# Optimization experiments

Measured on AMD Instinct MI355X. Metric: run time of the kernel, lower is better.

The kernel has to match this reference:

```python
import jax, jax.numpy as jnp
import numpy as np
import math

D_MODEL = 1024
N_HEADS = 16
HEAD_DIM = D_MODEL // N_HEADS


def get_slopes(n_heads: int) -> jnp.ndarray:
    def pow2_slopes(n):
        start = 2.0 ** (-8.0 / n)
        return np.array([start * start ** i for i in range(n)], dtype=np.float32)
    if math.log2(n_heads).is_integer():
        return jnp.asarray(pow2_slopes(n_heads))
    closest = 2 ** math.floor(math.log2(n_heads))
    base = pow2_slopes(closest)
    extra = pow2_slopes(2 * closest)[::2][: n_heads - closest]
    return jnp.asarray(np.concatenate([base, extra]))


def setup_inputs() -> dict:
    key = jax.random.key(0)
    ks = jax.random.split(key, 9)
    s = 1.0 / math.sqrt(D_MODEL)
    x = jax.random.normal(ks[0], (2, 2048, D_MODEL), dtype=jnp.float32)
    q_w = jax.random.uniform(ks[1], (D_MODEL, D_MODEL), jnp.float32, -s, s)
    q_b = jax.random.uniform(ks[2], (D_MODEL,), jnp.float32, -s, s)
    k_w = jax.random.uniform(ks[3], (D_MODEL, D_MODEL), jnp.float32, -s, s)
    k_b = jax.random.uniform(ks[4], (D_MODEL,), jnp.float32, -s, s)
    v_w = jax.random.uniform(ks[5], (D_MODEL, D_MODEL), jnp.float32, -s, s)
    v_b = jax.random.uniform(ks[6], (D_MODEL,), jnp.float32, -s, s)
    o_w = jax.random.uniform(ks[7], (D_MODEL, D_MODEL), jnp.float32, -s, s)
    o_b = jax.random.uniform(ks[8], (D_MODEL,), jnp.float32, -s, s)
    return {"x": x, "q_w": q_w, "q_b": q_b, "k_w": k_w, "k_b": k_b,
            "v_w": v_w, "v_b": v_b, "o_w": o_w, "o_b": o_b}


def reference(x, q_w, q_b, k_w, k_b, v_w, v_b, o_w, o_b):
    B, S, D = x.shape
    H, hd = N_HEADS, HEAD_DIM
    # torch Linear: y = x @ W.T + b
    Q = (x @ q_w.T + q_b).reshape(B, S, H, hd).transpose(0, 2, 1, 3)  # [B,H,S,hd]
    K = (x @ k_w.T + k_b).reshape(B, S, H, hd).transpose(0, 2, 1, 3)
    V = (x @ v_w.T + v_b).reshape(B, S, H, hd).transpose(0, 2, 1, 3)
    scores = jnp.einsum('bhqd,bhkd->bhqk', Q, K) / math.sqrt(hd)
    # ALiBi bias: slopes[h] * (k_pos - q_pos)
    pos = jnp.arange(S)
    rel = (pos[None, :] - pos[:, None]).astype(scores.dtype)  # [S,S]
    slopes = get_slopes(H)
    scores = scores + slopes[None, :, None, None] * rel[None, None, :, :]
    # causal mask
    causal = pos[None, :] <= pos[:, None]  # [S,S] True where allowed
    scores = jnp.where(causal[None, None], scores, -jnp.inf)
    attn = jax.nn.softmax(scores, axis=-1)  # dropout=0 (eval)
    out = jnp.einsum('bhqk,bhkd->bhqd', attn, V)
    out = out.transpose(0, 2, 1, 3).reshape(B, S, D)
    return out @ o_w.T + o_b
```

## Files before the change

### kernel.cpp

```cpp
#include <hip/hip_runtime.h>
#include <hip/hip_bf16.h>

typedef __attribute__((ext_vector_type(8))) short short8;
typedef __attribute__((ext_vector_type(4))) float float4v;
typedef __attribute__((ext_vector_type(4))) short short4v;
typedef __attribute__((ext_vector_type(4))) unsigned int uint4v;
typedef __attribute__((ext_vector_type(2))) unsigned int uint2v;

#define B_ 2
#define S_ 2048
#define D_ 1024
#define H_ 16
#define HD_ 64
#define M_ 4096
#define LOG2E 1.442695040888963f

__device__ __forceinline__ unsigned short f2bf(float f) {
  unsigned int u = __builtin_bit_cast(unsigned int, f);
  u += 0x7fffu + ((u >> 16) & 1u);
  return (unsigned short)(u >> 16);
}

__device__ __forceinline__ unsigned int pkbf(float a, float b) {
  __hip_bfloat162 h = __float22bfloat162_rn(make_float2(a, b));
  unsigned int u;
  __builtin_memcpy(&u, &h, sizeof(u));
  return u;
}

__device__ __forceinline__ void gload_lds16(const void* g, void* l) {
  __builtin_amdgcn_global_load_lds(
      (const __attribute__((address_space(1))) void*)g,
      (__attribute__((address_space(3))) void*)l, 16, 0, 0);
}

__global__ __launch_bounds__(256, 4) void cvt_kernel(
    const float* __restrict__ x,  const float* __restrict__ qw,
    const float* __restrict__ kw, const float* __restrict__ vw,
    const float* __restrict__ ow, unsigned short* __restrict__ dst)
{
  const int seg = blockIdx.y;
  const float* src;
  size_t doff;
  if (seg < 4)       { src = x + (size_t)seg * 1048576; doff = (size_t)seg * 1048576; }
  else if (seg == 4) { src = qw; doff = 4194304u; }
  else if (seg == 5) { src = kw; doff = 4194304u + 1048576u; }
  else if (seg == 6) { src = vw; doff = 4194304u + 2097152u; }
  else               { src = ow; doff = 4194304u + 3145728u; }
  const size_t i = ((size_t)blockIdx.x * 256 + threadIdx.x) * 4;
  float4v v = *(const float4v*)(src + i);
  short4v p;
#pragma unroll
  for (int r = 0; r < 4; ++r) p[r] = (short)f2bf(v[r]);
  *(short4v*)(dst + doff + i) = p;
}

template <int TN>
__global__ __launch_bounds__(256, 2) void gemm_kernel(
    const unsigned short* __restrict__ X,
    const unsigned short* __restrict__ W0, const unsigned short* __restrict__ W1,
    const unsigned short* __restrict__ W2,
    const float* __restrict__ Bi0, const float* __restrict__ Bi1,
    const float* __restrict__ Bi2,
    unsigned short* O0, unsigned short* O1, unsigned short* O2,
    float* OutF, int md0, int md1, int md2)
{
  constexpr int NJ = TN / 32;
  const int z = blockIdx.z;
  const unsigned short* W  = (z == 0) ? W0  : ((z == 1) ? W1  : W2);
  const float* Bi          = (z == 0) ? Bi0 : ((z == 1) ? Bi1 : Bi2);
  unsigned short* Out      = (z == 0) ? O0  : ((z == 1) ? O1  : O2);
  const int mode           = (z == 0) ? md0 : ((z == 1) ? md1 : md2);

  __shared__ __align__(16) char smem[8192 + TN * 64];
  __shared__ __align__(16) float tb[32 * 132];
  char* As = smem;
  char* Bs = smem + 8192;

  const int t = threadIdx.x, l = t & 63;
  const int w = t >> 6, lr = l & 15, lg = l >> 4;
  const int n0 = blockIdx.x * TN, m0 = blockIdx.y * 128;
  const int wm = (w >> 1) * 64, wn = (w & 1) * (TN / 2);

  float4v acc[4][NJ];
#pragma unroll
  for (int i = 0; i < 4; ++i)
#pragma unroll
    for (int j = 0; j < NJ; ++j) acc[i][j] = (float4v){0.f, 0.f, 0.f, 0.f};

  const int c0 = t, c1 = t + 256;
  const int r0 = c0 >> 2, k80 = (c0 & 3) * 8;
  const int r1 = c1 >> 2, k81 = (c1 & 3) * 8;

  for (int k0 = 0; k0 < 1024; k0 += 32) {
    __syncthreads();
    gload_lds16(X + (size_t)(m0 + r0) * 1024 + k0 + k80, As + c0 * 16);
    gload_lds16(X + (size_t)(m0 + r1) * 1024 + k0 + k81, As + c1 * 16);
    gload_lds16(W + (size_t)(n0 + r0) * 1024 + k0 + k80, Bs + c0 * 16);
    if (TN == 128)
      gload_lds16(W + (size_t)(n0 + r1) * 1024 + k0 + k81, Bs + c1 * 16);
    __syncthreads();

    short8 af[4], bfr[NJ];
#pragma unroll
    for (int i = 0; i < 4; ++i)
      af[i] = *(const short8*)(As + (wm + i * 16 + lr) * 64 + lg * 16);
#pragma unroll
    for (int j = 0; j < NJ; ++j)
      bfr[j] = *(const short8*)(Bs + (wn + j * 16 + lr) * 64 + lg * 16);
#pragma unroll
    for (int i = 0; i < 4; ++i)
#pragma unroll
      for (int j = 0; j < NJ; ++j)
        acc[i][j] = __builtin_amdgcn_mfma_f32_16x16x32_bf16(af[i], bfr[j], acc[i][j], 0, 0, 0);
  }

  float bv[NJ];
#pragma unroll
  for (int j = 0; j < NJ; ++j) bv[j] = Bi[n0 + wn + j * 16 + lr];

  if constexpr (TN == 128) {
    if (mode == 1) {
      const int rbase = (w >> 1) * 16;
      const int row16 = t >> 3, chunk = t & 7;
#pragma unroll
      for (int i = 0; i < 4; ++i) {
#pragma unroll
        for (int j = 0; j < 4; ++j)
#pragma unroll
          for (int r = 0; r < 4; ++r)
            tb[(rbase + lg * 4 + r) * 132 + wn + j * 16 + lr] = acc[i][j][r] + bv[j];
        __syncthreads();
        const int grow = m0 + ((row16 < 16) ? (i * 16 + row16) : (64 + i * 16 + row16 - 16));
        const int b = grow >> 11, sl = grow & 2047;
        const int colg = n0 + chunk * 16;
        const int hh = colg >> 6, d0 = colg & 63;
        float4v v4[4];
#pragma unroll
        for (int q = 0; q < 4; ++q)
          v4[q] = *(const float4v*)(tb + row16 * 132 + chunk * 16 + q * 4);
        uint4v lo, hi;
#pragma unroll
        for (int q = 0; q < 2; ++q) {
          lo[q * 2]     = pkbf(v4[q][0], v4[q][1]);
          lo[q * 2 + 1] = pkbf(v4[q][2], v4[q][3]);
          hi[q * 2]     = pkbf(v4[q + 2][0], v4[q + 2][1]);
          hi[q * 2 + 1] = pkbf(v4[q + 2][2], v4[q + 2][3]);
        }
        unsigned short* dst = Out + ((size_t)(b * H_ + hh) * S_ + sl) * HD_ + d0;
        *(short8*)dst = __builtin_bit_cast(short8, lo);
        *(short8*)(dst + 8) = __builtin_bit_cast(short8, hi);
        __syncthreads();
      }
      return;
    }
    if (mode == 2) {
#pragma unroll
      for (int i = 0; i < 4; ++i) {
        const int rowb = m0 + wm + i * 16 + lg * 4;
#pragma unroll
        for (int j = 0; j < 4; ++j) {
          const int col = n0 + wn + j * 16 + lr;
          const int b = rowb >> 11, s = rowb & 2047;
          const int hh = col >> 6, d = col & 63;
          uint2v pk2;
          pk2[0] = pkbf(acc[i][j][0] + bv[j], acc[i][j][1] + bv[j]);
          pk2[1] = pkbf(acc[i][j][2] + bv[j], acc[i][j][3] + bv[j]);
          *(short4v*)(Out + ((size_t)(b * H_ + hh) * HD_ + d) * S_ + s) =
              __builtin_bit_cast(short4v, pk2);
        }
      }
      return;
    }
  }
#pragma unroll
  for (int i = 0; i < 4; ++i) {
    const int rowb = m0 + wm + i * 16 + lg * 4;
#pragma unroll
    for (int j = 0; j < NJ; ++j) {
      const int col = n0 + wn + j * 16 + lr;
#pragma unroll
      for (int r = 0; r < 4; ++r)
        OutF[(size_t)(rowb + r) * 1024 + col] = acc[i][j][r] + bv[j];
    }
  }
}

__global__ __launch_bounds__(256, 2) void attn_kernel(
    const unsigned short* __restrict__ Q, const unsigned short* __restrict__ K,
    const unsigned short* __restrict__ VT, unsigned short* __restrict__ O)
{
  __shared__ __align__(16) char smem[32768];

  const int t = threadIdx.x, l = t & 63;
  const int w = t >> 6, lr = l & 15, lg = l >> 4;
  const int bh = blockIdx.x;
  const int it = 31 - (int)blockIdx.y;
  const int h = bh & 15;

  const unsigned short* qbp = Q + (size_t)bh * S_ * HD_;
  const unsigned short* kbp = K + (size_t)bh * S_ * HD_;
  const unsigned short* vbp = VT + (size_t)bh * HD_ * S_;

  const float slope2 = __builtin_amdgcn_exp2f(-0.5f * (float)(h + 1)) * LOG2E;
  const float qksc = 0.125f * LOG2E;

  const int g0 = t, g1 = t + 256;
  const int sr0 = g0 >> 3, sc0 = (g0 & 7) ^ (sr0 & 7);
  const int sr1 = g1 >> 3, sc1 = (g1 & 7) ^ (sr1 & 7);

  const int fchunk = ((4 + lg) ^ (lr & 7)) * 16;
  const int fchunk0 = ((lg) ^ (lr & 7)) * 16;

  const int qrow = it * 64 + w * 16;
  const int qpos = qrow + lr;

  short8 ones;
#pragma unroll
  for (int e = 0; e < 8; ++e) ones[e] = (short)0x3F80;

  short8 qf[2];
#pragma unroll
  for (int ks = 0; ks < 2; ++ks)
    qf[ks] = *(const short8*)(qbp + (size_t)(qrow + lr) * HD_ + ks * 32 + lg * 8);

  float4v o_acc[4], l_acc;
#pragma unroll
  for (int dt = 0; dt < 4; ++dt) o_acc[dt] = (float4v){0.f, 0.f, 0.f, 0.f};
  l_acc = (float4v){0.f, 0.f, 0.f, 0.f};
  float m_st = -1e30f;

  gload_lds16(kbp + (size_t)sr0 * HD_ + sc0 * 8, smem + g0 * 16);
  gload_lds16(kbp + (size_t)sr1 * HD_ + sc1 * 8, smem + g1 * 16);
  gload_lds16(vbp + (size_t)sr0 * S_ + sc0 * 8, smem + 16384 + g0 * 16);
  gload_lds16(vbp + (size_t)sr1 * S_ + sc1 * 8, smem + 16384 + g1 * 16);
  __syncthreads();

  for (int j = 0; j <= it; ++j) {
    const int cur = j & 1;
    char* Ks = smem + (cur ? 8192 : 0);
    char* Vs = smem + 16384 + (cur ? 8192 : 0);
    if (j < it) {
      char* Kn = smem + (cur ? 0 : 8192);
      char* Vn = smem + 16384 + (cur ? 0 : 8192);
      const int jn = j + 1;
      gload_lds16(kbp + (size_t)(jn * 64 + sr0) * HD_ + sc0 * 8, Kn + g0 * 16);
      gload_lds16(kbp + (size_t)(jn * 64 + sr1) * HD_ + sc1 * 8, Kn + g1 * 16);
      gload_lds16(vbp + (size_t)sr0 * S_ + jn * 64 + sc0 * 8, Vn + g0 * 16);
      gload_lds16(vbp + (size_t)sr1 * S_ + jn * 64 + sc1 * 8, Vn + g1 * 16);
    }

    float4v s_acc[4];
#pragma unroll
    for (int nj = 0; nj < 4; ++nj) {
      s_acc[nj] = (float4v){0.f, 0.f, 0.f, 0.f};
      short8 kf0 = *(const short8*)(Ks + (nj * 16 + lr) * 128 + fchunk0);
      s_acc[nj] = __builtin_amdgcn_mfma_f32_16x16x32_bf16(kf0, qf[0], s_acc[nj], 0, 0, 0);
      short8 kf1 = *(const short8*)(Ks + (nj * 16 + lr) * 128 + fchunk);
      s_acc[nj] = __builtin_amdgcn_mfma_f32_16x16x32_bf16(kf1, qf[1], s_acc[nj], 0, 0, 0);
    }

#pragma unroll
    for (int nj = 0; nj < 4; ++nj) {
      const float cb = slope2 * (float)(j * 64 + nj * 16 + lg * 4);
#pragma unroll
      for (int r = 0; r < 4; ++r)
        s_acc[nj][r] = s_acc[nj][r] * qksc + (cb + slope2 * (float)r);
    }
    if (j == it) {
#pragma unroll
      for (int nj = 0; nj < 4; ++nj)
#pragma unroll
        for (int r = 0; r < 4; ++r) {
          const int kpos = j * 64 + nj * 16 + lg * 4 + r;
          if (kpos > qpos) s_acc[nj][r] = -1e30f;
        }
    }

    float mx = s_acc[0][0];
#pragma unroll
    for (int nj = 0; nj < 4; ++nj)
#pragma unroll
      for (int r = 0; r < 4; ++r) mx = fmaxf(mx, s_acc[nj][r]);
    mx = fmaxf(mx, __shfl_xor(mx, 16, 64));
    mx = fmaxf(mx, __shfl_xor(mx, 32, 64));
    const float mn = fmaxf(m_st, mx);
    const float alpha = __builtin_amdgcn_exp2f(m_st - mn);
    m_st = mn;
#pragma unroll
    for (int nj = 0; nj < 4; ++nj)
#pragma unroll
      for (int r = 0; r < 4; ++r)
        s_acc[nj][r] = __builtin_amdgcn_exp2f(s_acc[nj][r] - mn);
#pragma unroll
    for (int dt = 0; dt < 4; ++dt)
#pragma unroll
      for (int r = 0; r < 4; ++r) o_acc[dt][r] *= alpha;
#pragma unroll
    for (int r = 0; r < 4; ++r) l_acc[r] *= alpha;

    short8 pT[2];
#pragma unroll
    for (int njp = 0; njp < 2; ++njp) {
      uint4v u;
      u[0] = pkbf(s_acc[njp * 2][0], s_acc[njp * 2][1]);
      u[1] = pkbf(s_acc[njp * 2][2], s_acc[njp * 2][3]);
      u[2] = pkbf(s_acc[njp * 2 + 1][0], s_acc[njp * 2 + 1][1]);
      u[3] = pkbf(s_acc[njp * 2 + 1][2], s_acc[njp * 2 + 1][3]);
      pT[njp] = __builtin_bit_cast(short8, u);
    }

    l_acc = __builtin_amdgcn_mfma_f32_16x16x32_bf16(ones, pT[0], l_acc, 0, 0, 0);
    l_acc = __builtin_amdgcn_mfma_f32_16x16x32_bf16(ones, pT[1], l_acc, 0, 0, 0);

    const int vcl = lr & 7;
#pragma unroll
    for (int dt = 0; dt < 4; ++dt) {
      const char* rowp = Vs + (dt * 16 + lr) * 128;
#pragma unroll
      for (int njp = 0; njp < 2; ++njp) {
        const int cA = ((njp * 4 + (lg >> 1)) ^ vcl) * 16 + (lg & 1) * 8;
        const int cB = ((njp * 4 + 2 + (lg >> 1)) ^ vcl) * 16 + (lg & 1) * 8;
        short4v v0 = *(const short4v*)(rowp + cA);
        short4v v1 = *(const short4v*)(rowp + cB);
        short8 vf8;
#pragma unroll
        for (int e = 0; e < 4; ++e) { vf8[e] = v0[e]; vf8[e + 4] = v1[e]; }
        o_acc[dt] = __builtin_amdgcn_mfma_f32_16x16x32_bf16(vf8, pT[njp], o_acc[dt], 0, 0, 0);
      }
    }
    __syncthreads();
  }

  char* tw = smem + w * 4416;
#pragma unroll
  for (int dt = 0; dt < 4; ++dt)
#pragma unroll
    for (int r = 0; r < 4; ++r)
      *(float*)(tw + ((dt * 16 + lg * 4 + r) * 17 + lr) * 4) = o_acc[dt][r];
  if (lg == 0) *(float*)(tw + 4352 + lr * 4) = l_acc[0];

  const int q2 = l >> 2, dbase = (l & 3) * 16;
  const float invl = 1.0f / *(const float*)(tw + 4352 + q2 * 4);
  uint4v os0, os1;
#pragma unroll
  for (int k = 0; k < 8; ++k) {
    const float va = *(const float*)(tw + ((dbase + 2 * k) * 17 + q2) * 4) * invl;
    const float vb = *(const float*)(tw + ((dbase + 2 * k + 1) * 17 + q2) * 4) * invl;
    if (k < 4) os0[k] = pkbf(va, vb); else os1[k - 4] = pkbf(va, vb);
  }
  const int brow = (bh >> 4) * S_;
  unsigned short* op = O + (size_t)(brow + qrow + q2) * 1024 + h * 64 + dbase;
  *(short8*)op = __builtin_bit_cast(short8, os0);
  *(short8*)(op + 8) = __builtin_bit_cast(short8, os1);
}

extern "C" void kernel_launch(void* const* d_in, const int* in_sizes, int n_in,
                              void* d_out, int out_size, void* d_ws, size_t ws_size,
                              hipStream_t stream) {
  (void)in_sizes; (void)n_in; (void)out_size; (void)ws_size;
  const float* x  = (const float*)d_in[0];
  const float* qw = (const float*)d_in[1];
  const float* qb = (const float*)d_in[2];
  const float* kw = (const float*)d_in[3];
  const float* kb = (const float*)d_in[4];
  const float* vw = (const float*)d_in[5];
  const float* vb = (const float*)d_in[6];
  const float* ow = (const float*)d_in[7];
  const float* ob = (const float*)d_in[8];
  float* out = (float*)d_out;

  unsigned short* xb  = (unsigned short*)d_ws;
  unsigned short* qwb = xb  + (size_t)M_ * D_;
  unsigned short* kwb = qwb + (size_t)D_ * D_;
  unsigned short* vwb = kwb + (size_t)D_ * D_;
  unsigned short* owb = vwb + (size_t)D_ * D_;
  unsigned short* qws = owb + (size_t)D_ * D_;
  unsigned short* kws = qws + (size_t)M_ * D_;
  unsigned short* vws = kws + (size_t)M_ * D_;
  unsigned short* aws = vws + (size_t)M_ * D_;

  cvt_kernel<<<dim3(1024, 8), dim3(256), 0, stream>>>(x, qw, kw, vw, ow, xb);
  gemm_kernel<128><<<dim3(8, 32, 3), dim3(256), 0, stream>>>(
      xb, qwb, kwb, vwb, qb, kb, vb, qws, kws, vws, out, 1, 1, 2);
  attn_kernel<<<dim3(32, 32), dim3(256), 0, stream>>>(qws, kws, vws, aws);
  gemm_kernel<64><<<dim3(16, 32, 1), dim3(256), 0, stream>>>(
      aws, owb, owb, owb, ob, ob, ob, aws, aws, aws, out, 0, 0, 0);
}
```

Before: 185.3 us.

## Lazy softmax rescale, hoisted ALiBi bias, permuted V layout for 16-byte loads

The V projection epilogue now permutes sequence positions within each 32-key group, so the attention loop can read each V fragment with one 16-byte LDS load instead of two 8-byte loads plus a register shuffle. The per-block ALiBi bias is hoisted into a precomputed per-lane table plus a running offset that is folded into the running max. Rescaling of the output and denominator accumulators is skipped unless some lane's max grows by more than a threshold, in the style of FA4 lazy rescaling. The max reduction uses three-input max ops. The lazy rescale adds a wave-level vote and a branch, and it relies on a bounded exp2 growth for fp32 and bf16 range safety.

```diff
diff --git a/kernel.cpp b/kernel.cpp
--- a/kernel.cpp
+++ b/kernel.cpp
@@ -26,6 +26,10 @@
   unsigned int u;
   __builtin_memcpy(&u, &h, sizeof(u));
   return u;
+}
+
+__device__ __forceinline__ float max3f(float a, float b, float c) {
+  return fmaxf(fmaxf(a, b), c);
 }
 
 __device__ __forceinline__ void gload_lds16(const void* g, void* l) {
@@ -163,10 +167,13 @@
           const int col = n0 + wn + j * 16 + lr;
           const int b = rowb >> 11, s = rowb & 2047;
           const int hh = col >> 6, d = col & 63;
+          const int gI = (s >> 2) & 7;
+          const int gP = ((gI & 3) << 1) | (gI >> 2);
+          const int sN = (s & ~31) | (gP << 2);
           uint2v pk2;
           pk2[0] = pkbf(acc[i][j][0] + bv[j], acc[i][j][1] + bv[j]);
           pk2[1] = pkbf(acc[i][j][2] + bv[j], acc[i][j][3] + bv[j]);
-          *(short4v*)(Out + ((size_t)(b * H_ + hh) * HD_ + d) * S_ + s) =
+          *(short4v*)(Out + ((size_t)(b * H_ + hh) * HD_ + d) * S_ + sN) =
               __builtin_bit_cast(short4v, pk2);
         }
       }
@@ -224,10 +231,21 @@
   for (int ks = 0; ks < 2; ++ks)
     qf[ks] = *(const short8*)(qbp + (size_t)(qrow + lr) * HD_ + ks * 32 + lg * 8);
 
+  float kb[16];
+#pragma unroll
+  for (int nj = 0; nj < 4; ++nj)
+#pragma unroll
+    for (int r = 0; r < 4; ++r)
+      kb[nj * 4 + r] = slope2 * (float)(nj * 16 + lg * 4 + r);
+  float jb = 0.0f;
+  const float jbstep = slope2 * 64.0f;
+
+  const float4v z4 = (float4v){0.f, 0.f, 0.f, 0.f};
+
   float4v o_acc[4], l_acc;
 #pragma unroll
-  for (int dt = 0; dt < 4; ++dt) o_acc[dt] = (float4v){0.f, 0.f, 0.f, 0.f};
-  l_acc = (float4v){0.f, 0.f, 0.f, 0.f};
+  for (int dt = 0; dt < 4; ++dt) o_acc[dt] = z4;
+  l_acc = z4;
   float m_st = -1e30f;
 
   gload_lds16(kbp + (size_t)sr0 * HD_ + sc0 * 8, smem + g0 * 16);
@@ -235,6 +253,8 @@
   gload_lds16(vbp + (size_t)sr0 * S_ + sc0 * 8, smem + 16384 + g0 * 16);
   gload_lds16(vbp + (size_t)sr1 * S_ + sc1 * 8, smem + 16384 + g1 * 16);
   __syncthreads();
+
+  const int vcl = lr & 7;
 
   for (int j = 0; j <= it; ++j) {
     const int cur = j & 1;
@@ -253,20 +273,17 @@
     float4v s_acc[4];
 #pragma unroll
     for (int nj = 0; nj < 4; ++nj) {
-      s_acc[nj] = (float4v){0.f, 0.f, 0.f, 0.f};
       short8 kf0 = *(const short8*)(Ks + (nj * 16 + lr) * 128 + fchunk0);
-      s_acc[nj] = __builtin_amdgcn_mfma_f32_16x16x32_bf16(kf0, qf[0], s_acc[nj], 0, 0, 0);
+      float4v t0 = __builtin_amdgcn_mfma_f32_16x16x32_bf16(kf0, qf[0], z4, 0, 0, 0);
       short8 kf1 = *(const short8*)(Ks + (nj * 16 + lr) * 128 + fchunk);
-      s_acc[nj] = __builtin_amdgcn_mfma_f32_16x16x32_bf16(kf1, qf[1], s_acc[nj], 0, 0, 0);
-    }
-
-#pragma unroll
-    for (int nj = 0; nj < 4; ++nj) {
-      const float cb = slope2 * (float)(j * 64 + nj * 16 + lg * 4);
+      s_acc[nj] = __builtin_amdgcn_mfma_f32_16x16x32_bf16(kf1, qf[1], t0, 0, 0, 0);
+    }
+
+#pragma unroll
+    for (int nj = 0; nj < 4; ++nj)
 #pragma unroll
       for (int r = 0; r < 4; ++r)
-        s_acc[nj][r] = s_acc[nj][r] * qksc + (cb + slope2 * (float)r);
-    }
+        s_acc[nj][r] = s_acc[nj][r] * qksc + kb[nj * 4 + r];
     if (j == it) {
 #pragma unroll
       for (int nj = 0; nj < 4; ++nj)
@@ -277,27 +294,34 @@
         }
     }
 
-    float mx = s_acc[0][0];
+    float a0 = max3f(s_acc[0][0], s_acc[0][1], s_acc[0][2]);
+    float a1 = max3f(s_acc[0][3], s_acc[1][0], s_acc[1][1]);
+    float a2 = max3f(s_acc[1][2], s_acc[1][3], s_acc[2][0]);
+    float a3 = max3f(s_acc[2][1], s_acc[2][2], s_acc[2][3]);
+    float a4 = max3f(s_acc[3][0], s_acc[3][1], s_acc[3][2]);
+    float b0 = max3f(a0, a1, a2);
+    float b1 = max3f(a3, a4, s_acc[3][3]);
+    float mxt = fmaxf(b0, b1);
+    mxt = fmaxf(mxt, __shfl_xor(mxt, 16, 64));
+    mxt = fmaxf(mxt, __shfl_xor(mxt, 32, 64));
+    const float mx = mxt + jb;
+    if (__any(mx > m_st + 8.0f)) {
+      const float mn = fmaxf(m_st, mx);
+      const float alpha = __builtin_amdgcn_exp2f(m_st - mn);
+      m_st = mn;
+#pragma unroll
+      for (int dt = 0; dt < 4; ++dt)
+#pragma unroll
+        for (int r = 0; r < 4; ++r) o_acc[dt][r] *= alpha;
+#pragma unroll
+      for (int r = 0; r < 4; ++r) l_acc[r] *= alpha;
+    }
+    const float c1 = m_st - jb;
 #pragma unroll
     for (int nj = 0; nj < 4; ++nj)
 #pragma unroll
-      for (int r = 0; r < 4; ++r) mx = fmaxf(mx, s_acc[nj][r]);
-    mx = fmaxf(mx, __shfl_xor(mx, 16, 64));
-    mx = fmaxf(mx, __shfl_xor(mx, 32, 64));
-    const float mn = fmaxf(m_st, mx);
-    const float alpha = __builtin_amdgcn_exp2f(m_st - mn);
-    m_st = mn;
-#pragma unroll
-    for (int nj = 0; nj < 4; ++nj)
-#pragma unroll
       for (int r = 0; r < 4; ++r)
-        s_acc[nj][r] = __builtin_amdgcn_exp2f(s_acc[nj][r] - mn);
-#pragma unroll
-    for (int dt = 0; dt < 4; ++dt)
-#pragma unroll
-      for (int r = 0; r < 4; ++r) o_acc[dt][r] *= alpha;
-#pragma unroll
-    for (int r = 0; r < 4; ++r) l_acc[r] *= alpha;
+        s_acc[nj][r] = __builtin_amdgcn_exp2f(s_acc[nj][r] - c1);
 
     short8 pT[2];
 #pragma unroll
@@ -313,22 +337,16 @@
     l_acc = __builtin_amdgcn_mfma_f32_16x16x32_bf16(ones, pT[0], l_acc, 0, 0, 0);
     l_acc = __builtin_amdgcn_mfma_f32_16x16x32_bf16(ones, pT[1], l_acc, 0, 0, 0);
 
-    const int vcl = lr & 7;
 #pragma unroll
     for (int dt = 0; dt < 4; ++dt) {
       const char* rowp = Vs + (dt * 16 + lr) * 128;
 #pragma unroll
       for (int njp = 0; njp < 2; ++njp) {
-        const int cA = ((njp * 4 + (lg >> 1)) ^ vcl) * 16 + (lg & 1) * 8;
-        const int cB = ((njp * 4 + 2 + (lg >> 1)) ^ vcl) * 16 + (lg & 1) * 8;
-        short4v v0 = *(const short4v*)(rowp + cA);
-        short4v v1 = *(const short4v*)(rowp + cB);
-        short8 vf8;
-#pragma unroll
-        for (int e = 0; e < 4; ++e) { vf8[e] = v0[e]; vf8[e + 4] = v1[e]; }
+        short8 vf8 = *(const short8*)(rowp + (((njp * 4 + lg) ^ vcl) << 4));
         o_acc[dt] = __builtin_amdgcn_mfma_f32_16x16x32_bf16(vf8, pT[njp], o_acc[dt], 0, 0, 0);
       }
     }
+    jb += jbstep;
     __syncthreads();
   }
 
```

Result: faster. 181.1 us (-2.2%).
